# Optimization experiments

Hardware: AMD Instinct MI355X
Metric: run time of the kernel (lower is better)

## Reference

```python
import jax, jax.numpy as jnp
import numpy as np

VOCAB, TYPES, D0, D1, D2 = 30522, 2, 64, 768, 64
MAXOFF = 64
GLOB = 64
EPS = 1e-12


def _rel_pos_ids_np(S, M):
    # toeplitz(c, r): T[i,j] = c[i-j] if i>=j else r[j-i]
    r = np.clip(np.arange(S), None, M - 1)
    c = np.clip(-np.arange(S), -M + 1, None)
    c = c.copy()
    c[1:] += 2 * M
    d = np.arange(S)[:, None] - np.arange(S)[None, :]
    return np.where(d >= 0, c[np.clip(d, 0, S - 1)], r[np.clip(-d, 0, S - 1)]).astype(np.int32)


def _ln(x):
    u = jnp.mean(x, axis=-1, keepdims=True)
    s = jnp.mean((x - u) ** 2, axis=-1, keepdims=True)
    return (x - u) / jnp.sqrt(s + EPS)


def setup_inputs() -> dict:
    key = jax.random.key(0)
    ks = jax.random.split(key, 9)
    B, S = 8, 512
    std = 0.02
    return {
        "tok_seq": jax.random.randint(ks[0], (B, S), 0, VOCAB, dtype=jnp.int32),
        "tok_type_ids": jax.random.randint(ks[1], (B, S), 0, TYPES, dtype=jnp.int32),
        "W_word": jax.random.normal(ks[2], (VOCAB, D1), jnp.float32) * std,
        "W_type": jax.random.normal(ks[3], (TYPES, D1), jnp.float32) * std,
        "W_abs": jax.random.normal(ks[4], (512, D1), jnp.float32) * std,
        "W_rel": jax.random.normal(ks[5], (2 * MAXOFF + 2, D2), jnp.float32) * std,
        "W_glob": jax.random.normal(ks[6], (GLOB, D0), jnp.float32) * std,
        "W_diag": jax.random.normal(ks[7], (D2, D1), jnp.float32) * std,
        "b_diag": jnp.zeros((D2,), jnp.float32),
    }


def reference(tok_seq, tok_type_ids, W_word, W_type, W_abs, W_rel, W_glob, W_diag, b_diag):
    B, S = tok_seq.shape
    # unary predicates: word + type + absolute position embeddings
    embd1 = W_word[tok_seq] + W_type[tok_type_ids] + W_abs[jnp.arange(S)][None]  # [B,S,D1]

    # relative-position ids (static toeplitz), masked by token-type segments
    rpe = jnp.asarray(_rel_pos_ids_np(S, MAXOFF))[None]                 # [1,S,S]
    same = (tok_type_ids[:, :, None] == tok_type_ids[:, None, :]).astype(jnp.int32)
    rpe = rpe * same + (1 - same) * MAXOFF                              # [B,S,S]
    rpe = rpe.at[:, 0, 1:].set(2 * MAXOFF)
    rpe = rpe.at[:, 1:, 0].set(2 * MAXOFF + 1)
    embd2 = W_rel[rpe]                                                  # [B,S,S,D2]

    # diag link: project embd1 and scatter onto the (i,i) diagonal of embd2
    diag2 = embd1 @ W_diag.T + b_diag                                   # [B,S,D2]
    ar = jnp.arange(S)
    embd2 = embd2.at[:, ar, ar, :].add(diag2)

    # global predicates
    embd0 = jnp.broadcast_to(W_glob[None], (B, GLOB, D0))

    embd0 = _ln(embd0)
    embd1 = _ln(embd1)
    embd2 = _ln(embd2)
    return (embd0, embd1, embd2)
```

## Files before the change

### kernel.cpp

```cpp
#include <hip/hip_runtime.h>
#include <hip/hip_bf16.h>

#define S_ 512
#define D1_ 768

typedef unsigned int v4u __attribute__((ext_vector_type(4)));


__device__ __forceinline__ float wsum(float v) {
#pragma unroll
    for (int o = 32; o; o >>= 1) v += __shfl_xor(v, o);
    return v;
}

__global__ __launch_bounds__(64) void k_small(const float* __restrict__ Wg,
                                              const float* __restrict__ Wr,
                                              float* __restrict__ out0,
                                              float* __restrict__ table) {
    int t = threadIdx.x;
    int bid = blockIdx.x;
    float v = (bid < 64) ? Wg[bid * 64 + t] : Wr[(bid - 64) * 64 + t];
    float m = wsum(v) * (1.f / 64.f);
    float d = v - m;
    float q = wsum(d * d) * (1.f / 64.f);
    float o = d * rsqrtf(q + 1e-12f);
    if (bid < 64) {
#pragma unroll
        for (int b = 0; b < 8; b++) out0[b * 4096 + bid * 64 + t] = o;
    } else {
        table[(bid - 64) * 64 + t] = o;
    }
}

__global__ __launch_bounds__(256) void k_embd1(const int* __restrict__ tok,
                                               const int* __restrict__ tty,
                                               const float* __restrict__ Ww,
                                               const float* __restrict__ Wt,
                                               const float* __restrict__ Wa,
                                               float* __restrict__ out1,
                                               float* __restrict__ rawout) {
    __shared__ float ssum[4], ssq[4];
    int t = threadIdx.x;
    int bs = blockIdx.x;
    int s = bs & (S_ - 1);
    size_t wrow = (size_t)tok[bs] * D1_;
    int trow = tty[bs] * D1_;
    int arow = s * D1_;
    float v0 = Ww[wrow + t]       + Wt[trow + t]       + Wa[arow + t];
    float v1 = Ww[wrow + t + 256] + Wt[trow + t + 256] + Wa[arow + t + 256];
    float v2 = Ww[wrow + t + 512] + Wt[trow + t + 512] + Wa[arow + t + 512];
    float ls = v0 + v1 + v2;
    float lq = v0 * v0 + v1 * v1 + v2 * v2;
    float s1 = wsum(ls), q1 = wsum(lq);
    int w = t >> 6;
    if ((t & 63) == 0) { ssum[w] = s1; ssq[w] = q1; }
    __syncthreads();
    float Sa = ssum[0] + ssum[1] + ssum[2] + ssum[3];
    float Qa = ssq[0] + ssq[1] + ssq[2] + ssq[3];
    float mean = Sa * (1.f / 768.f);
    float var = Qa * (1.f / 768.f) - mean * mean;
    float rstd = rsqrtf(var + 1e-12f);
    size_t ob = (size_t)bs * D1_;
    out1[ob + t]       = (v0 - mean) * rstd;
    out1[ob + t + 256] = (v1 - mean) * rstd;
    out1[ob + t + 512] = (v2 - mean) * rstd;
    rawout[ob + t] = v0;
    rawout[ob + t + 256] = v1;
    rawout[ob + t + 512] = v2;
}

__global__ __launch_bounds__(256) void k_diagmm(const float* __restrict__ rawS,
                                                const float* __restrict__ Wd,
                                                const float* __restrict__ bd,
                                                const float* __restrict__ Wr,
                                                float* __restrict__ diagLN) {
    __shared__ float rawT[1024];
    __shared__ float wdT[64 * 65];
    int t = threadIdx.x;
    int r0 = blockIdx.x * 16;
    int c = t & 63, rq = t >> 6;
    float a0 = 0.f, a1 = 0.f, a2 = 0.f, a3 = 0.f;
    for (int k0 = 0; k0 < 768; k0 += 64) {
        for (int x = t; x < 1024; x += 256)
            rawT[x] = rawS[(r0 + (x >> 6)) * 768 + k0 + (x & 63)];
        for (int x = t; x < 4096; x += 256) {
            int cc = x >> 6, kk = x & 63;
            wdT[kk * 65 + cc] = Wd[cc * 768 + k0 + kk];
        }
        __syncthreads();
#pragma unroll 16
        for (int kk = 0; kk < 64; kk++) {
            float wv = wdT[kk * 65 + c];
            a0 += rawT[rq * 64 + kk] * wv;
            a1 += rawT[(rq + 4) * 64 + kk] * wv;
            a2 += rawT[(rq + 8) * 64 + kk] * wv;
            a3 += rawT[(rq + 12) * 64 + kk] * wv;
        }
        __syncthreads();
    }
    float bb = bd[c];
    float w0 = Wr[c];
    float acc[4] = {a0, a1, a2, a3};
#pragma unroll
    for (int m = 0; m < 4; m++) {
        float v = acc[m] + bb + w0;
        float mean = wsum(v) * (1.f / 64.f);
        float d = v - mean;
        float q = wsum(d * d) * (1.f / 64.f);
        diagLN[(r0 + rq + 4 * m) * 64 + c] = d * rsqrtf(q + 1e-12f);
    }
}

__global__ __launch_bounds__(256) void k_embd2(const int* __restrict__ tty,
                                               const v4u* __restrict__ table,
                                               const v4u* __restrict__ diagLN,
                                               v4u* __restrict__ out2) {
    __shared__ int ty[S_];
    int t = threadIdx.x;
    int bi = blockIdx.x;
    int b = bi >> 9, i = bi & (S_ - 1);
    for (int j = t; j < S_; j += 256) ty[j] = tty[b * S_ + j];
    __syncthreads();
    int ti = ty[i];
    int sub = t & 15;
    int jbase = t >> 4;
    size_t obase = (size_t)bi * (S_ * 16);
    const v4u* drow = diagLN + (size_t)bi * 16;
#pragma unroll 8
    for (int it = 0; it < 32; it++) {
        int j = it * 16 + jbase;
        int d = i - j;
        const v4u* src;
        if (d == 0)           src = drow;
        else if (i == 0)      src = table + 128 * 16;
        else if (j == 0)      src = table + 129 * 16;
        else if (ty[j] != ti) src = table + 64 * 16;
        else if (d > 0)       src = table + (128 - (d < 63 ? d : 63)) * 16;
        else { int nd = -d;   src = table + (nd < 63 ? nd : 63) * 16; }
        __builtin_nontemporal_store(src[sub], &out2[obase + (size_t)j * 16 + sub]);
    }
}

extern "C" void kernel_launch(void* const* d_in, const int* in_sizes, int n_in,
                              void* d_out, int out_size, void* d_ws, size_t ws_size,
                              hipStream_t stream) {
    const int* tok  = (const int*)d_in[0];
    const int* tty  = (const int*)d_in[1];
    const float* Ww = (const float*)d_in[2];
    const float* Wt = (const float*)d_in[3];
    const float* Wa = (const float*)d_in[4];
    const float* Wr = (const float*)d_in[5];
    const float* Wg = (const float*)d_in[6];
    const float* Wd = (const float*)d_in[7];
    const float* bd = (const float*)d_in[8];

    float* out  = (float*)d_out;
    float* out0 = out;
    float* out1 = out + 32768;
    float* out2 = out + 3178496;

    float* table  = (float*)d_ws;
    float* diagLN = (float*)((char*)d_ws + 65536);
    float* rawws  = (float*)((char*)d_ws + 2097152);

    hipLaunchKernelGGL(k_small, dim3(194), dim3(64), 0, stream, Wg, Wr, out0, table);
    hipLaunchKernelGGL(k_embd1, dim3(4096), dim3(256), 0, stream,
                       tok, tty, Ww, Wt, Wa, out1, rawws);
    hipLaunchKernelGGL(k_diagmm, dim3(256), dim3(256), 0, stream,
                       rawws, Wd, bd, Wr, diagLN);
    hipLaunchKernelGGL(k_embd2, dim3(4096), dim3(256), 0, stream,
                       tty, (const v4u*)table, (const v4u*)diagLN, (v4u*)out2);
}
```

Baseline: 653.2 us.

## Pre-transpose diag weight into float4 layout and restructure diag matmul

New measurement: 628.8 us. 3.7% less time.

```diff
diff --git a/kernel.cpp b/kernel.cpp
--- a/kernel.cpp
+++ b/kernel.cpp
@@ -15,10 +15,18 @@
 
 __global__ __launch_bounds__(64) void k_small(const float* __restrict__ Wg,
                                               const float* __restrict__ Wr,
+                                              const float* __restrict__ Wd,
                                               float* __restrict__ out0,
-                                              float* __restrict__ table) {
+                                              float* __restrict__ table,
+                                              float4* __restrict__ wdT4) {
     int t = threadIdx.x;
     int bid = blockIdx.x;
+    if (bid >= 194) {
+        int g = bid - 194;
+        float4 v = *(const float4*)(Wd + (size_t)t * D1_ + 4 * g);
+        wdT4[g * 64 + t] = v;
+        return;
+    }
     float v = (bid < 64) ? Wg[bid * 64 + t] : Wr[(bid - 64) * 64 + t];
     float m = wsum(v) * (1.f / 64.f);
     float d = v - m;
@@ -70,44 +78,42 @@
 }
 
 __global__ __launch_bounds__(256) void k_diagmm(const float* __restrict__ rawS,
-                                                const float* __restrict__ Wd,
+                                                const float4* __restrict__ wdT4,
                                                 const float* __restrict__ bd,
                                                 const float* __restrict__ Wr,
                                                 float* __restrict__ diagLN) {
-    __shared__ float rawT[1024];
-    __shared__ float wdT[64 * 65];
+    __shared__ float rawT[8 * D1_];
     int t = threadIdx.x;
-    int r0 = blockIdx.x * 16;
+    int r0 = blockIdx.x * 8;
+    for (int x = t; x < 8 * D1_; x += 256)
+        rawT[x] = rawS[(size_t)r0 * D1_ + x];
+    __syncthreads();
     int c = t & 63, rq = t >> 6;
-    float a0 = 0.f, a1 = 0.f, a2 = 0.f, a3 = 0.f;
-    for (int k0 = 0; k0 < 768; k0 += 64) {
-        for (int x = t; x < 1024; x += 256)
-            rawT[x] = rawS[(r0 + (x >> 6)) * 768 + k0 + (x & 63)];
-        for (int x = t; x < 4096; x += 256) {
-            int cc = x >> 6, kk = x & 63;
-            wdT[kk * 65 + cc] = Wd[cc * 768 + k0 + kk];
-        }
-        __syncthreads();
-#pragma unroll 16
-        for (int kk = 0; kk < 64; kk++) {
-            float wv = wdT[kk * 65 + c];
-            a0 += rawT[rq * 64 + kk] * wv;
-            a1 += rawT[(rq + 4) * 64 + kk] * wv;
-            a2 += rawT[(rq + 8) * 64 + kk] * wv;
-            a3 += rawT[(rq + 12) * 64 + kk] * wv;
-        }
-        __syncthreads();
+    const float4* ra4 = (const float4*)&rawT[rq * D1_];
+    const float4* rb4 = (const float4*)&rawT[(rq + 4) * D1_];
+    float a0 = 0.f, a1 = 0.f;
+#pragma unroll 4
+    for (int g = 0; g < 192; g++) {
+        float4 w = wdT4[g * 64 + c];
+        float4 x = ra4[g];
+        float4 y = rb4[g];
+        a0 += x.x * w.x + x.y * w.y + x.z * w.z + x.w * w.w;
+        a1 += y.x * w.x + y.y * w.y + y.z * w.z + y.w * w.w;
     }
-    float bb = bd[c];
-    float w0 = Wr[c];
-    float acc[4] = {a0, a1, a2, a3};
-#pragma unroll
-    for (int m = 0; m < 4; m++) {
-        float v = acc[m] + bb + w0;
+    float base = bd[c] + Wr[c];
+    {
+        float v = a0 + base;
         float mean = wsum(v) * (1.f / 64.f);
         float d = v - mean;
         float q = wsum(d * d) * (1.f / 64.f);
-        diagLN[(r0 + rq + 4 * m) * 64 + c] = d * rsqrtf(q + 1e-12f);
+        diagLN[(r0 + rq) * 64 + c] = d * rsqrtf(q + 1e-12f);
+    }
+    {
+        float v = a1 + base;
+        float mean = wsum(v) * (1.f / 64.f);
+        float d = v - mean;
+        float q = wsum(d * d) * (1.f / 64.f);
+        diagLN[(r0 + rq + 4) * 64 + c] = d * rsqrtf(q + 1e-12f);
     }
 }
 
@@ -161,13 +167,15 @@
 
     float* table  = (float*)d_ws;
     float* diagLN = (float*)((char*)d_ws + 65536);
+    float4* wdT4  = (float4*)((char*)d_ws + 1114112);
     float* rawws  = (float*)((char*)d_ws + 2097152);
 
-    hipLaunchKernelGGL(k_small, dim3(194), dim3(64), 0, stream, Wg, Wr, out0, table);
+    hipLaunchKernelGGL(k_small, dim3(386), dim3(64), 0, stream,
+                       Wg, Wr, Wd, out0, table, wdT4);
     hipLaunchKernelGGL(k_embd1, dim3(4096), dim3(256), 0, stream,
                        tok, tty, Ww, Wt, Wa, out1, rawws);
-    hipLaunchKernelGGL(k_diagmm, dim3(256), dim3(256), 0, stream,
-                       rawws, Wd, bd, Wr, diagLN);
+    hipLaunchKernelGGL(k_diagmm, dim3(512), dim3(256), 0, stream,
+                       rawws, wdT4, bd, Wr, diagLN);
     hipLaunchKernelGGL(k_embd2, dim3(4096), dim3(256), 0, stream,
                        tty, (const v4u*)table, (const v4u*)diagLN, (v4u*)out2);
 }
```
